# Performance work log

Hardware: AMD Instinct MI355X
Metric: run time of the kernel (lower is better)

Reference implementation:

```python
import jax, jax.numpy as jnp
import numpy as np

B, S, E = 4, 2048, 512
Q, FFN = 8, 2048


def setup_inputs() -> dict:
    key = jax.random.key(0)
    k_x, k_th, k_w1, k_w2 = jax.random.split(key, 4)
    x = jax.random.normal(k_x, (B, S, E), dtype=jnp.float32)
    # trainable RY angles, one per wire
    theta = jax.random.normal(k_th, (Q,), dtype=jnp.float32)
    W1 = jax.random.normal(k_w1, (Q, FFN), dtype=jnp.float32) / np.sqrt(Q)
    b1 = jnp.zeros((FFN,), dtype=jnp.float32)
    W2 = jax.random.normal(k_w2, (FFN, E), dtype=jnp.float32) / np.sqrt(FFN)
    b2 = jnp.zeros((E,), dtype=jnp.float32)
    return {"x": x, "theta": theta, "W1": W1, "b1": b1, "W2": W2, "b2": b2}


def reference(x, theta, W1, b1, W2, b2):
    # Quantum circuit: |0> -> RX(x_i) -> RY(theta_i) -> <Z> per wire.
    # No entangling gates, so the 8-qubit state factorizes; simulate each
    # qubit's 2 complex amplitudes, batched over all tokens & wires at once.
    n_wires = theta.shape[0]
    xq = x[..., :n_wires]                     # encoder uses input_idx 0..7: [B,S,Q]
    # RX(x)|0> = cos(x/2)|0> - i sin(x/2)|1>
    a = jnp.cos(xq * 0.5).astype(jnp.complex64)
    b = (-1j) * jnp.sin(xq * 0.5).astype(jnp.complex64)
    # RY(theta) = [[c,-s],[s,c]], c=cos(theta/2), s=sin(theta/2)
    c = jnp.cos(theta * 0.5).astype(jnp.complex64)
    s = jnp.sin(theta * 0.5).astype(jnp.complex64)
    a2 = c * a - s * b
    b2_ = s * a + c * b
    # <Z> = |amp0|^2 - |amp1|^2  -> [B,S,Q]
    z = (jnp.abs(a2) ** 2 - jnp.abs(b2_) ** 2).astype(x.dtype)
    # dropout is identity at inference
    h = jax.nn.relu(jnp.einsum('bsq,qf->bsf', z, W1) + b1)
    return jnp.einsum('bsf,fe->bse', h, W2) + b2
```

## Files before the change

### kernel.cpp

```cpp
#include <hip/hip_runtime.h>
#include <hip/hip_bf16.h>

typedef __bf16 bf16_t;
typedef __bf16 bf16x4 __attribute__((ext_vector_type(4)));
typedef __bf16 bf16x8 __attribute__((ext_vector_type(8)));
typedef float f32x4 __attribute__((ext_vector_type(4)));

#define M_TOT 8192
#define N_TOT 512
#define K_TOT 2048
#define E_TOT 512
#define NT    32

__device__ __forceinline__ bf16x8 zero8() {
    bf16x8 v;
#pragma unroll
    for (int i = 0; i < 8; ++i) v[i] = (bf16_t)0.0f;
    return v;
}

__global__ __launch_bounds__(256)
void prep4_kernel(const float* __restrict__ x,
                  const float* __restrict__ theta,
                  const float* __restrict__ W1,
                  const float* __restrict__ b1,
                  const float* __restrict__ W2,
                  bf16_t* __restrict__ W2t,
                  bf16_t* __restrict__ zb,
                  bf16_t* __restrict__ W1p)
{
    const int b = blockIdx.x;
    if (b < 256) {
        __shared__ bf16_t T[64][66];
        const int k0 = (b >> 3) * 64;
        const int n0 = (b & 7) * 64;
        const int kl = threadIdx.x >> 4;
        const int n4 = threadIdx.x & 15;
#pragma unroll
        for (int i = 0; i < 4; ++i) {
            int k = kl + i * 16;
            float4 v = *(const float4*)(W2 + (size_t)(k0 + k) * N_TOT + n0 + n4 * 4);
            T[n4 * 4 + 0][k] = (bf16_t)v.x;
            T[n4 * 4 + 1][k] = (bf16_t)v.y;
            T[n4 * 4 + 2][k] = (bf16_t)v.z;
            T[n4 * 4 + 3][k] = (bf16_t)v.w;
        }
        __syncthreads();
        const int nl = threadIdx.x >> 4;
        const int k4 = threadIdx.x & 15;
#pragma unroll
        for (int i = 0; i < 4; ++i) {
            int n = nl + i * 16;
            bf16x4 v;
            v[0] = T[n][k4 * 4 + 0];
            v[1] = T[n][k4 * 4 + 1];
            v[2] = T[n][k4 * 4 + 2];
            v[3] = T[n][k4 * 4 + 3];
            *(bf16x4*)(W2t + (size_t)(n0 + n) * K_TOT + k0 + k4 * 4) = v;
        }
    } else if (b < 288) {
        const int m = (b - 256) * 256 + threadIdx.x;
        float4 x0 = *(const float4*)(x + (size_t)m * E_TOT);
        float4 x1 = *(const float4*)(x + (size_t)m * E_TOT + 4);
        float xs[8] = {x0.x, x0.y, x0.z, x0.w, x1.x, x1.y, x1.z, x1.w};
        bf16x8 lo;
#pragma unroll
        for (int q = 0; q < 8; ++q)
            lo[q] = (bf16_t)(__builtin_cosf(theta[q]) * __builtin_cosf(xs[q]));
        bf16x8 hi = zero8();
        hi[0] = (bf16_t)1.0f;
        *(bf16x8*)(zb + (size_t)m * 16)     = lo;
        *(bf16x8*)(zb + (size_t)m * 16 + 8) = hi;
    } else {
        const int d  = (b - 288) * 256 + threadIdx.x;
        const int c  = d >> 5;
        const int dd = d & 31;
        const int p  = dd >> 4;
        const int rr = dd & 15;
        const int f  = c * 32 + ((rr >> 2) << 3) + (p << 2) + (rr & 3);
        bf16x8 lo;
#pragma unroll
        for (int q = 0; q < 8; ++q)
            lo[q] = (bf16_t)W1[(size_t)q * K_TOT + f];
        bf16x8 hi = zero8();
        hi[0] = (bf16_t)b1[f];
        *(bf16x8*)(W1p + (size_t)d * 16)     = lo;
        *(bf16x8*)(W1p + (size_t)d * 16 + 8) = hi;
    }
}

__device__ __forceinline__ void load_B(const bf16_t* __restrict__ W2t, int n_base,
                                       int k0, int t, uint4 gv[2]) {
#pragma unroll
    for (int j = 0; j < 2; ++j) {
        int s = t + j * 512;
        int n = s >> 3;
        int g = (s & 7) ^ (n & 7);
        gv[j] = *(const uint4*)(W2t + (size_t)(n_base + n) * K_TOT + k0 + g * 8);
    }
}
__device__ __forceinline__ void write_B(bf16_t* Bb, int t, const uint4 gv[2]) {
#pragma unroll
    for (int j = 0; j < 2; ++j) {
        int s = t + j * 512;
        *(uint4*)(Bb + (s >> 3) * 64 + (s & 7) * 8) = gv[j];
    }
}

__device__ __forceinline__ void load_wf(const bf16_t* __restrict__ W1p, int k0,
                                        int l15, int lq, bf16x8 wf[4]) {
#pragma unroll
    for (int i = 0; i < 4; ++i) wf[i] = zero8();
    if (lq < 2) {
        const int base = (k0 >> 5) * 2;
#pragma unroll
        for (int i = 0; i < 4; ++i)
            wf[i] = *(const bf16x8*)(W1p + (size_t)((base + i) * 16 + l15) * 16 + lq * 8);
    }
}

__device__ __forceinline__ void compute_tile(const bf16_t* Bb, const bf16x8 wf[4],
                                             const bf16x8 zfrag[2],
                                             int wn, int l15, int lq,
                                             f32x4 acc[2][4]) {
    bf16x8 bfr[2][4];
#pragma unroll
    for (int c = 0; c < 2; ++c)
#pragma unroll
        for (int nt = 0; nt < 4; ++nt) {
            int r = wn * 64 + nt * 16 + l15;
            int s = (c * 4 + lq) ^ (r & 7);
            bfr[c][nt] = *(const bf16x8*)(Bb + r * 64 + s * 8);
        }

    bf16x8 af[2][2];
#pragma unroll
    for (int mt = 0; mt < 2; ++mt)
#pragma unroll
        for (int c = 0; c < 2; ++c) {
            f32x4 h0 = (f32x4){0.f, 0.f, 0.f, 0.f};
            f32x4 h1 = (f32x4){0.f, 0.f, 0.f, 0.f};
            h0 = __builtin_amdgcn_mfma_f32_16x16x32_bf16(wf[c * 2 + 0], zfrag[mt], h0, 0, 0, 0);
            h1 = __builtin_amdgcn_mfma_f32_16x16x32_bf16(wf[c * 2 + 1], zfrag[mt], h1, 0, 0, 0);
            bf16x8 a;
#pragma unroll
            for (int r = 0; r < 4; ++r) {
                a[r]     = (bf16_t)fmaxf(h0[r], 0.f);
                a[r + 4] = (bf16_t)fmaxf(h1[r], 0.f);
            }
            af[mt][c] = a;
        }

#pragma unroll
    for (int c = 0; c < 2; ++c)
#pragma unroll
        for (int mt = 0; mt < 2; ++mt)
#pragma unroll
            for (int nt = 0; nt < 4; ++nt)
                acc[mt][nt] = __builtin_amdgcn_mfma_f32_16x16x32_bf16(
                    af[mt][c], bfr[c][nt], acc[mt][nt], 0, 0, 0);
}

__global__ __launch_bounds__(512, 2)
void ffq_gemm_kernel(const bf16_t* __restrict__ zb,
                     const bf16_t* __restrict__ W1p,
                     const bf16_t* __restrict__ W2t,
                     const float* __restrict__ b2,
                     float* __restrict__ out)
{
    __shared__ bf16_t Blds[2][128 * 64];

    const int t = threadIdx.x;
    const int w = t >> 6, l = t & 63;
    const int m_base = blockIdx.y * 128;
    const int n_base = blockIdx.x * 128;
    const int wm = w >> 1, wn = w & 1;
    const int l15 = l & 15, lq = l >> 4;

    bf16x8 zfrag[2];
#pragma unroll
    for (int mt = 0; mt < 2; ++mt) {
        zfrag[mt] = zero8();
        if (lq < 2)
            zfrag[mt] = *(const bf16x8*)(zb + (size_t)(m_base + wm * 32 + mt * 16 + l15) * 16 + lq * 8);
    }

    f32x4 acc[2][4];
#pragma unroll
    for (int mt = 0; mt < 2; ++mt)
#pragma unroll
        for (int nt = 0; nt < 4; ++nt)
            acc[mt][nt] = (f32x4){0.f, 0.f, 0.f, 0.f};

    uint4 gv[2];
    bf16x8 wfA[4], wfB[4];

    load_B(W2t, n_base, 0, t, gv);
    load_wf(W1p, 0, l15, lq, wfA);
    write_B(Blds[0], t, gv);

    for (int it = 0; it < NT; it += 2) {
        __syncthreads();
        load_B(W2t, n_base, (it + 1) * 64, t, gv);
        load_wf(W1p, (it + 1) * 64, l15, lq, wfB);
        compute_tile(Blds[0], wfA, zfrag, wn, l15, lq, acc);
        write_B(Blds[1], t, gv);

        __syncthreads();
        const bool more = (it + 2 < NT);
        if (more) {
            load_B(W2t, n_base, (it + 2) * 64, t, gv);
            load_wf(W1p, (it + 2) * 64, l15, lq, wfA);
        }
        compute_tile(Blds[1], wfB, zfrag, wn, l15, lq, acc);
        if (more) write_B(Blds[0], t, gv);
    }

#pragma unroll
    for (int nt = 0; nt < 4; ++nt) {
        int col = n_base + wn * 64 + nt * 16 + l15;
        float bias = b2[col];
#pragma unroll
        for (int mt = 0; mt < 2; ++mt) {
#pragma unroll
            for (int r = 0; r < 4; ++r) {
                int row = m_base + wm * 32 + mt * 16 + lq * 4 + r;
                out[(size_t)row * N_TOT + col] = acc[mt][nt][r] + bias;
            }
        }
    }
}

extern "C" void kernel_launch(void* const* d_in, const int* in_sizes, int n_in,
                              void* d_out, int out_size, void* d_ws, size_t ws_size,
                              hipStream_t stream) {
    const float* x     = (const float*)d_in[0];
    const float* theta = (const float*)d_in[1];
    const float* W1    = (const float*)d_in[2];
    const float* b1    = (const float*)d_in[3];
    const float* W2    = (const float*)d_in[4];
    const float* b2    = (const float*)d_in[5];
    float* out = (float*)d_out;

    const size_t W2T_BYTES = (size_t)N_TOT * K_TOT * sizeof(bf16_t);
    const size_t ZB_BYTES  = (size_t)M_TOT * 16 * sizeof(bf16_t);

    bf16_t* W2t = (bf16_t*)d_ws;
    bf16_t* zb  = (bf16_t*)((char*)d_ws + W2T_BYTES);
    bf16_t* W1p = (bf16_t*)((char*)d_ws + W2T_BYTES + ZB_BYTES);

    prep4_kernel<<<296, 256, 0, stream>>>(x, theta, W1, b1, W2, W2t, zb, W1p);

    dim3 grid(N_TOT / 128, M_TOT / 128);
    ffq_gemm_kernel<<<grid, 512, 0, stream>>>(zb, W1p, W2t, b2, out);
}
```

Measured before the change: 128.2 us.

## Shrink GEMM block to 128x64 with 4 waves and 128-deep K stages

Changes the second GEMM block tile from 128x128 with 8 waves to 128x64 with 4 waves, doubling the grid to 512 blocks. Each pipeline stage now loads a 128-wide K segment (two 64-wide subtiles) per barrier, halving the number of syncthreads. W1 fragments are loaded inside the stage instead of being prefetched a step ahead. The goal is better CU occupancy and fewer barriers, at the cost of recomputing the first-layer hidden activations twice as often across N blocks and loading the zb/W1p data more often.

After: 107.6 us. 16.0% less time.

```diff
diff --git a/kernel.cpp b/kernel.cpp
--- a/kernel.cpp
+++ b/kernel.cpp
@@ -10,7 +10,7 @@
 #define N_TOT 512
 #define K_TOT 2048
 #define E_TOT 512
-#define NT    32
+#define NSEG  16
 
 __device__ __forceinline__ bf16x8 zero8() {
     bf16x8 v;
@@ -90,20 +90,25 @@
 }
 
 __device__ __forceinline__ void load_B(const bf16_t* __restrict__ W2t, int n_base,
-                                       int k0, int t, uint4 gv[2]) {
-#pragma unroll
-    for (int j = 0; j < 2; ++j) {
-        int s = t + j * 512;
-        int n = s >> 3;
-        int g = (s & 7) ^ (n & 7);
-        gv[j] = *(const uint4*)(W2t + (size_t)(n_base + n) * K_TOT + k0 + g * 8);
-    }
-}
-__device__ __forceinline__ void write_B(bf16_t* Bb, int t, const uint4 gv[2]) {
-#pragma unroll
-    for (int j = 0; j < 2; ++j) {
-        int s = t + j * 512;
-        *(uint4*)(Bb + (s >> 3) * 64 + (s & 7) * 8) = gv[j];
+                                       int k0, int t, uint4 gv[4]) {
+#pragma unroll
+    for (int j = 0; j < 4; ++j) {
+        int s    = t + j * 256;
+        int tile = s >> 9;
+        int n    = (s >> 3) & 63;
+        int g    = (s & 7) ^ (n & 7);
+        gv[j] = *(const uint4*)(W2t + (size_t)(n_base + n) * K_TOT
+                                + k0 + tile * 64 + g * 8);
+    }
+}
+__device__ __forceinline__ void write_B(bf16_t* Bb, int t, const uint4 gv[4]) {
+#pragma unroll
+    for (int j = 0; j < 4; ++j) {
+        int s    = t + j * 256;
+        int tile = s >> 9;
+        int n    = (s >> 3) & 63;
+        int seg  = s & 7;
+        *(uint4*)(Bb + tile * 4096 + n * 64 + seg * 8) = gv[j];
     }
 }
 
@@ -121,14 +126,14 @@
 
 __device__ __forceinline__ void compute_tile(const bf16_t* Bb, const bf16x8 wf[4],
                                              const bf16x8 zfrag[2],
-                                             int wn, int l15, int lq,
+                                             int l15, int lq,
                                              f32x4 acc[2][4]) {
     bf16x8 bfr[2][4];
 #pragma unroll
     for (int c = 0; c < 2; ++c)
 #pragma unroll
         for (int nt = 0; nt < 4; ++nt) {
-            int r = wn * 64 + nt * 16 + l15;
+            int r = nt * 16 + l15;
             int s = (c * 4 + lq) ^ (r & 7);
             bfr[c][nt] = *(const bf16x8*)(Bb + r * 64 + s * 8);
         }
@@ -161,20 +166,20 @@
                     af[mt][c], bfr[c][nt], acc[mt][nt], 0, 0, 0);
 }
 
-__global__ __launch_bounds__(512, 2)
+__global__ __launch_bounds__(256, 2)
 void ffq_gemm_kernel(const bf16_t* __restrict__ zb,
                      const bf16_t* __restrict__ W1p,
                      const bf16_t* __restrict__ W2t,
                      const float* __restrict__ b2,
                      float* __restrict__ out)
 {
-    __shared__ bf16_t Blds[2][128 * 64];
+    __shared__ bf16_t Blds[2][2 * 64 * 64];
 
     const int t = threadIdx.x;
     const int w = t >> 6, l = t & 63;
     const int m_base = blockIdx.y * 128;
-    const int n_base = blockIdx.x * 128;
-    const int wm = w >> 1, wn = w & 1;
+    const int n_base = blockIdx.x * 64;
+    const int wm = w;
     const int l15 = l & 15, lq = l >> 4;
 
     bf16x8 zfrag[2];
@@ -192,33 +197,29 @@
         for (int nt = 0; nt < 4; ++nt)
             acc[mt][nt] = (f32x4){0.f, 0.f, 0.f, 0.f};
 
-    uint4 gv[2];
-    bf16x8 wfA[4], wfB[4];
+    uint4 gv[4];
 
     load_B(W2t, n_base, 0, t, gv);
-    load_wf(W1p, 0, l15, lq, wfA);
     write_B(Blds[0], t, gv);
 
-    for (int it = 0; it < NT; it += 2) {
+    for (int s = 0; s < NSEG; ++s) {
+        const int cur = s & 1;
         __syncthreads();
-        load_B(W2t, n_base, (it + 1) * 64, t, gv);
-        load_wf(W1p, (it + 1) * 64, l15, lq, wfB);
-        compute_tile(Blds[0], wfA, zfrag, wn, l15, lq, acc);
-        write_B(Blds[1], t, gv);
-
-        __syncthreads();
-        const bool more = (it + 2 < NT);
-        if (more) {
-            load_B(W2t, n_base, (it + 2) * 64, t, gv);
-            load_wf(W1p, (it + 2) * 64, l15, lq, wfA);
-        }
-        compute_tile(Blds[1], wfB, zfrag, wn, l15, lq, acc);
-        if (more) write_B(Blds[0], t, gv);
+        if (s + 1 < NSEG) load_B(W2t, n_base, (s + 1) * 128, t, gv);
+
+#pragma unroll
+        for (int tt = 0; tt < 2; ++tt) {
+            bf16x8 wf[4];
+            load_wf(W1p, s * 128 + tt * 64, l15, lq, wf);
+            compute_tile(Blds[cur] + tt * 4096, wf, zfrag, l15, lq, acc);
+        }
+
+        if (s + 1 < NSEG) write_B(Blds[1 - cur], t, gv);
     }
 
 #pragma unroll
     for (int nt = 0; nt < 4; ++nt) {
-        int col = n_base + wn * 64 + nt * 16 + l15;
+        int col = n_base + nt * 16 + l15;
         float bias = b2[col];
 #pragma unroll
         for (int mt = 0; mt < 2; ++mt) {
@@ -251,6 +252,6 @@
 
     prep4_kernel<<<296, 256, 0, stream>>>(x, theta, W1, b1, W2, W2t, zb, W1p);
 
-    dim3 grid(N_TOT / 128, M_TOT / 128);
-    ffq_gemm_kernel<<<grid, 512, 0, stream>>>(zb, W1p, W2t, b2, out);
-}
+    dim3 grid(N_TOT / 64, M_TOT / 128);
+    ffq_gemm_kernel<<<grid, 256, 0, stream>>>(zb, W1p, W2t, b2, out);
+}
```
